# Kernel optimization log

Measured on AMD Instinct MI355X. Metric: run time of the kernel, lower is better.

The kernel has to match this reference:

```python
import jax, jax.numpy as jnp
import numpy as np

B, L, H, Di, N, K, R = 2, 512, 2048, 4096, 16, 4, 128


def setup_inputs() -> dict:
    key = jax.random.key(0)
    ks = jax.random.split(key, 8)
    s = 0.02
    inp = {
        "x": jax.random.normal(ks[0], (B, L, H), jnp.float32),
        "in_w": jax.random.normal(ks[1], (2 * Di, H), jnp.float32) * s,
        "in_b": jnp.zeros((2 * Di,), jnp.float32),
        "conv_w": jax.random.normal(ks[2], (Di, 1, K), jnp.float32) * s,  # depthwise conv weight
        "conv_b": jnp.zeros((Di,), jnp.float32),
        "xproj_w": jax.random.normal(ks[3], (R + 2 * N, Di), jnp.float32) * s,
        "dt_w": jax.random.normal(ks[4], (Di, R), jnp.float32) * s,
        "dt_b": jax.random.normal(ks[5], (Di,), jnp.float32) * 0.1,
        "A_log": jnp.log(jnp.broadcast_to(jnp.arange(1, N + 1, dtype=jnp.float32)[None, :], (Di, N))) + jnp.zeros((Di, N), jnp.float32),
        "D": jnp.ones((Di,), jnp.float32),
        "out_w": jax.random.normal(ks[6], (H, Di), jnp.float32) * s,
        "out_b": jnp.zeros((H,), jnp.float32),
    }
    return inp


def reference(x, in_w, in_b, conv_w, conv_b, xproj_w, dt_w, dt_b, A_log, D, out_w, out_b):
    silu = jax.nn.silu
    # in_proj -> split into hidden path and gate
    proj = x @ in_w.T + in_b                       # [B, L, 2*Di]
    h, gate = jnp.split(proj, 2, axis=-1)          # each [B, L, Di]
    # causal depthwise conv1d over time
    hc = jnp.transpose(h, (0, 2, 1))               # [B, Di, L]
    hc = jax.lax.conv_general_dilated(
        hc, conv_w, window_strides=(1,), padding=[(K - 1, 0)],
        dimension_numbers=("NCH", "OIH", "NCH"), feature_group_count=Di)
    hc = silu(hc + conv_b[None, :, None])          # [B, Di, L]
    hs = jnp.transpose(hc, (0, 2, 1))              # [B, L, Di]
    # input-dependent SSM parameters
    sp = hs @ xproj_w.T                            # [B, L, R + 2N]
    ts, Bm, Cm = sp[..., :R], sp[..., R:R + N], sp[..., R + N:]
    dt = jax.nn.softplus(ts @ dt_w.T + dt_b)       # [B, L, Di]
    A = -jnp.exp(A_log)                            # [Di, N]
    dA = jnp.exp(dt[..., None] * A[None, None])    # [B, L, Di, N]
    dBu = dt[..., None] * Bm[:, :, None, :] * hs[..., None]  # [B, L, Di, N]

    # selective scan: s_t = dA_t * s_{t-1} + dBu_t ; y_t = s_t . C_t
    def step(s, inputs):
        dA_t, dBu_t, C_t = inputs                  # [B,Di,N], [B,Di,N], [B,N]
        s = dA_t * s + dBu_t
        y = jnp.einsum("bdn,bn->bd", s, C_t)
        return s, y

    s0 = jnp.zeros((x.shape[0], Di, N), x.dtype)
    _, ys = jax.lax.scan(step, s0, (jnp.swapaxes(dA, 0, 1), jnp.swapaxes(dBu, 0, 1), jnp.swapaxes(Cm, 0, 1)))
    y = jnp.transpose(ys, (1, 0, 2))               # [B, L, Di]
    y = (y + hs * D) * silu(gate)
    return y @ out_w.T + out_b                     # [B, L, H]
```

## Files before the change

### kernel.cpp

```cpp
#include <hip/hip_runtime.h>
#include <hip/hip_bf16.h>

typedef __hip_bfloat16 bf16;
typedef _Float16 fp16;
typedef short bf16x8 __attribute__((ext_vector_type(8)));
typedef float f32x4 __attribute__((ext_vector_type(4)));
typedef _Float16 half8 __attribute__((ext_vector_type(8)));

#define BB 2
#define LL 512
#define HH 2048
#define DI 4096
#define NST 16
#define KK 4
#define RR 128
#define BLM (BB*LL)
#define CN 16
#define LC (LL/CN)
#define ZXP 16
#define ZOUT 4

enum { MODE_PROJ = 0, MODE_XPROJ = 1, MODE_DT = 2, MODE_OUT = 3 };

__device__ __forceinline__ float sigmoidf_(float x) { return 1.f / (1.f + __expf(-x)); }
__device__ __forceinline__ float softplusf_(float x) {
    return fmaxf(x, 0.f) + log1pf(__expf(-fabsf(x)));
}
__device__ __forceinline__ unsigned int bfpack(float a, float b) {
    __hip_bfloat162 h = __float22bfloat162_rn(make_float2(a, b));
    union { __hip_bfloat162 h; unsigned int u; } cv; cv.h = h;
    return cv.u;
}

typedef const __attribute__((address_space(1))) unsigned int* gas_t;
typedef __attribute__((address_space(3))) unsigned int* las_t;
__device__ __forceinline__ void gld16(const void* g, void* l) {
    __builtin_amdgcn_global_load_lds((gas_t)g, (las_t)l, 16, 0, 0);
}

__device__ __forceinline__ void cvt_seg(const float* s, bf16* d, int i) {
    float4 v = ((const float4*)s)[i];
    uint2 o; o.x = bfpack(v.x, v.y); o.y = bfpack(v.z, v.w);
    ((uint2*)d)[i] = o;
}

__global__ __launch_bounds__(256) void cvt_all(
    const float* __restrict__ s0, bf16* __restrict__ d0, int n0,
    const float* __restrict__ s1, bf16* __restrict__ d1, int n1,
    const float* __restrict__ s2, bf16* __restrict__ d2, int n2,
    const float* __restrict__ s3, bf16* __restrict__ d3, int n3)
{
    int i = blockIdx.x * 256 + threadIdx.x;
    int stride = gridDim.x * 256;
    int t1 = n0 + n1, t2 = t1 + n2, t3 = t2 + n3;
    for (; i < t3; i += stride) {
        if      (i < n0) cvt_seg(s0, d0, i);
        else if (i < t1) cvt_seg(s1, d1, i - n0);
        else if (i < t2) cvt_seg(s2, d2, i - t1);
        else             cvt_seg(s3, d3, i - t2);
    }
}

__global__ __launch_bounds__(256) void cvt_f32_bf16(
    const float* __restrict__ src, bf16* __restrict__ dst, int n4)
{
    int i = blockIdx.x * 256 + threadIdx.x;
    int stride = gridDim.x * 256;
    for (; i < n4; i += stride) cvt_seg(src, dst, i);
}

template<int BM, int BN, int MODE>
__global__ __launch_bounds__(256) void gemm_bf16(
    const bf16* __restrict__ A, const bf16* __restrict__ Bw,
    int N, int K, int lda, int ldb,
    const float* __restrict__ bias,
    float* __restrict__ outf, bf16* __restrict__ outh, bf16* __restrict__ outh2,
    fp16* __restrict__ s0, fp16* __restrict__ s1,
    fp16* __restrict__ s2, fp16* __restrict__ s3)
{
    __shared__ short sA[BM * 32];
    __shared__ short sB[BN * 32];
    const int tid = threadIdx.x;
    const int col0 = blockIdx.x * BN;
    const int row0 = blockIdx.y * BM;
    const int wave = tid >> 6;
    const int lane = tid & 63;
    constexpr int NJ = (BM == 64 || BN == 64) ? 2 : 4;
    const int wr = (BM == 128) ? ((wave >> 1) * 64) : 0;
    const int wc = (BM == 64) ? (wave * 32) : ((wave & 1) * (BN / 2));
    const int lr = lane & 15;
    const int kq = (lane >> 4) << 3;

    const int kpb = K / gridDim.z;
    const int kbeg = blockIdx.z * kpb;
    const int kend = kbeg + kpb;

    const int r0 = tid >> 2;
    const int kc = (tid & 3) << 3;

    f32x4 acc[4][NJ] = {};

    for (int k0 = kbeg; k0 < kend; k0 += 32) {
        #pragma unroll
        for (int p = 0; p < BM / 64; p++) {
            int r = r0 + p * 64;
            gld16(A + (size_t)(row0 + r) * lda + k0 + kc, &sA[r * 32 + kc]);
        }
        #pragma unroll
        for (int p = 0; p < BN / 64; p++) {
            int rr = r0 + p * 64;
            int nb = col0 + rr; if (nb > N - 1) nb = N - 1;
            gld16(Bw + (size_t)nb * ldb + k0 + kc, &sB[rr * 32 + kc]);
        }
        __syncthreads();
        bf16x8 af[4], bfr[NJ];
        #pragma unroll
        for (int i = 0; i < 4; i++)
            af[i] = *(const bf16x8*)(&sA[(wr + i * 16 + lr) * 32 + kq]);
        #pragma unroll
        for (int j = 0; j < NJ; j++)
            bfr[j] = *(const bf16x8*)(&sB[(wc + j * 16 + lr) * 32 + kq]);
        #pragma unroll
        for (int i = 0; i < 4; i++)
            #pragma unroll
            for (int j = 0; j < NJ; j++)
                acc[i][j] = __builtin_amdgcn_mfma_f32_16x16x32_bf16(af[i], bfr[j], acc[i][j], 0, 0, 0);
        __syncthreads();
    }

    fp16* oslice = nullptr;
    if (MODE == MODE_OUT) {
        int z = blockIdx.z;
        oslice = (z == 0) ? s0 : (z == 1) ? s1 : (z == 2) ? s2 : s3;
    }
    const int drow = (lane >> 4) << 2;
    const int dcol = lane & 15;
    #pragma unroll
    for (int i = 0; i < 4; i++) {
        #pragma unroll
        for (int j = 0; j < NJ; j++) {
            int n = col0 + wc + j * 16 + dcol;
            if (n >= N) continue;
            float bv = bias ? bias[n] : 0.f;
            #pragma unroll
            for (int r = 0; r < 4; r++) {
                int m = row0 + wr + i * 16 + drow + r;
                float v = acc[i][j][r];
                if (MODE == MODE_PROJ) {
                    v += bv;
                    if (n < DI) outh2[(size_t)m * DI + n] = (bf16)v;
                    else        outh[(size_t)m * DI + (n - DI)] = (bf16)v;
                } else if (MODE == MODE_XPROJ) {
                    outf[(size_t)blockIdx.z * (BLM * 160) + (size_t)m * 160 + n] = v;
                } else if (MODE == MODE_DT) {
                    outf[(size_t)m * DI + n] = softplusf_(v + bv);
                } else {
                    oslice[(size_t)m * HH + n] = (fp16)v;
                }
            }
        }
    }
}

__global__ __launch_bounds__(256) void reduce_sp(
    const float* __restrict__ spS, float* __restrict__ sp_f, bf16* __restrict__ ts_b)
{
    int i = blockIdx.x * 256 + threadIdx.x;
    int row = i / 40, c4 = (i % 40) * 4;
    float4 s = make_float4(0.f, 0.f, 0.f, 0.f);
    #pragma unroll
    for (int z = 0; z < ZXP; z++) {
        float4 v = *(const float4*)&spS[(size_t)z * (BLM * 160) + (size_t)row * 160 + c4];
        s.x += v.x; s.y += v.y; s.z += v.z; s.w += v.w;
    }
    *(float4*)&sp_f[(size_t)row * 160 + c4] = s;
    if (c4 < RR) {
        uint2 o; o.x = bfpack(s.x, s.y); o.y = bfpack(s.z, s.w);
        *(uint2*)&ts_b[(size_t)row * RR + c4] = o;
    }
}

__global__ __launch_bounds__(256) void reduce_out(
    const fp16* __restrict__ s0, const fp16* __restrict__ s1,
    const fp16* __restrict__ s2, const fp16* __restrict__ s3,
    const float* __restrict__ bias, float* __restrict__ out)
{
    int i = blockIdx.x * 256 + threadIdx.x;
    int c8 = (i & 255) << 3;
    half8 a = ((const half8*)s0)[i];
    half8 b = ((const half8*)s1)[i];
    half8 c = ((const half8*)s2)[i];
    half8 d = ((const half8*)s3)[i];
    float r[8];
    #pragma unroll
    for (int e = 0; e < 8; e++)
        r[e] = (float)a[e] + (float)b[e] + (float)c[e] + (float)d[e] + bias[c8 + e];
    ((float4*)out)[2 * i]     = make_float4(r[0], r[1], r[2], r[3]);
    ((float4*)out)[2 * i + 1] = make_float4(r[4], r[5], r[6], r[7]);
}

__global__ __launch_bounds__(256) void conv_silu(
    const bf16* __restrict__ h, const float* __restrict__ conv_w,
    const float* __restrict__ conv_b, bf16* __restrict__ hs_b)
{
    int idx = blockIdx.x * 256 + threadIdx.x;
    int d = idx & (DI - 1);
    int l = (idx >> 12) & (LL - 1);
    float acc = conv_b[d];
    #pragma unroll
    for (int k = 0; k < KK; k++) {
        int ls = l - (KK - 1) + k;
        if (ls >= 0) acc += (float)h[(size_t)idx + (size_t)(ls - l) * DI] * conv_w[d * KK + k];
    }
    float s = acc * sigmoidf_(acc);
    hs_b[idx] = (bf16)s;
}

__global__ __launch_bounds__(256) void scan_part1(
    const float* __restrict__ dtr, const float* __restrict__ sp,
    const bf16* __restrict__ hs_b, const float* __restrict__ A_log,
    float* __restrict__ P_ws, float* __restrict__ S_ws)
{
    int bid = blockIdx.x;
    int c  = bid & (CN - 1);
    int db = (bid >> 4) & (DI / 256 - 1);
    int b  = bid >> 8;
    int d  = db * 256 + threadIdx.x;

    float A[NST], P[NST], S[NST];
    #pragma unroll
    for (int n = 0; n < NST; n++) {
        A[n] = -__expf(A_log[d * NST + n]);
        P[n] = 1.f; S[n] = 0.f;
    }
    const float* spb = sp + (size_t)b * LL * 160;
    size_t base = (size_t)b * LL * DI + d;
    for (int l = c * LC; l < (c + 1) * LC; l++) {
        size_t off = base + (size_t)l * DI;
        float dtv = dtr[off];
        float hsv = (float)hs_b[off];
        float dh = dtv * hsv;
        #pragma unroll
        for (int n = 0; n < NST; n++) {
            float a  = __expf(dtv * A[n]);
            float Bn = spb[l * 160 + RR + n];
            S[n] = a * S[n] + dh * Bn;
            P[n] *= a;
        }
    }
    size_t o = ((size_t)((b * CN + c) * DI) + d) * NST;
    #pragma unroll
    for (int q = 0; q < 4; q++) {
        *(float4*)&P_ws[o + q * 4] = make_float4(P[q*4], P[q*4+1], P[q*4+2], P[q*4+3]);
        *(float4*)&S_ws[o + q * 4] = make_float4(S[q*4], S[q*4+1], S[q*4+2], S[q*4+3]);
    }
}

__global__ __launch_bounds__(256) void scan_part2(
    const float* __restrict__ dtr, const float* __restrict__ sp,
    const bf16* __restrict__ hs_b, const bf16* __restrict__ g_b,
    const float* __restrict__ A_log, const float* __restrict__ Dv,
    const float* __restrict__ P_ws, const float* __restrict__ S_ws,
    bf16* __restrict__ y_b)
{
    int bid = blockIdx.x;
    int c  = bid & (CN - 1);
    int db = (bid >> 4) & (DI / 256 - 1);
    int b  = bid >> 8;
    int d  = db * 256 + threadIdx.x;

    float s[NST];
    #pragma unroll
    for (int n = 0; n < NST; n++) s[n] = 0.f;
    for (int j = 0; j < c; j++) {
        size_t o = ((size_t)((b * CN + j) * DI) + d) * NST;
        #pragma unroll
        for (int q = 0; q < 4; q++) {
            float4 Pq = *(const float4*)&P_ws[o + q * 4];
            float4 Sq = *(const float4*)&S_ws[o + q * 4];
            s[q*4+0] = Pq.x * s[q*4+0] + Sq.x;
            s[q*4+1] = Pq.y * s[q*4+1] + Sq.y;
            s[q*4+2] = Pq.z * s[q*4+2] + Sq.z;
            s[q*4+3] = Pq.w * s[q*4+3] + Sq.w;
        }
    }

    float A[NST];
    #pragma unroll
    for (int n = 0; n < NST; n++) A[n] = -__expf(A_log[d * NST + n]);
    float Dd = Dv[d];

    const float* spb = sp + (size_t)b * LL * 160;
    size_t base = (size_t)b * LL * DI + d;
    for (int l = c * LC; l < (c + 1) * LC; l++) {
        size_t off = base + (size_t)l * DI;
        float dtv = dtr[off];
        float hsv = (float)hs_b[off];
        float dh = dtv * hsv;
        float y = 0.f;
        #pragma unroll
        for (int n = 0; n < NST; n++) {
            float a  = __expf(dtv * A[n]);
            float Bn = spb[l * 160 + RR + n];
            float Cn = spb[l * 160 + RR + NST + n];
            s[n] = a * s[n] + dh * Bn;
            y += s[n] * Cn;
        }
        float gv = (float)g_b[off];
        y_b[off] = (bf16)((y + hsv * Dd) * (gv * sigmoidf_(gv)));
    }
}

extern "C" void kernel_launch(void* const* d_in, const int* in_sizes, int n_in,
                              void* d_out, int out_size, void* d_ws, size_t ws_size,
                              hipStream_t stream)
{
    const float* x       = (const float*)d_in[0];
    const float* in_w    = (const float*)d_in[1];
    const float* in_b    = (const float*)d_in[2];
    const float* conv_w  = (const float*)d_in[3];
    const float* conv_b  = (const float*)d_in[4];
    const float* xproj_w = (const float*)d_in[5];
    const float* dt_w    = (const float*)d_in[6];
    const float* dt_b    = (const float*)d_in[7];
    const float* A_log   = (const float*)d_in[8];
    const float* Dv      = (const float*)d_in[9];
    const float* out_w   = (const float*)d_in[10];
    const float* out_b   = (const float*)d_in[11];
    float* out = (float*)d_out;

    char* ws = (char*)d_ws;
    const size_t MB = 1u << 20;
    bf16*  x_b    = (bf16*)(ws);
    float* spS    = (float*)(ws);
    float* P_ws   = (float*)(ws);
    float* S_ws   = (float*)(ws + 8 * MB);
    fp16*  oS2    = (fp16*)(ws);
    fp16*  oS3    = (fp16*)(ws + 4 * MB);
    bf16*  in_w_b = (bf16*)(ws + 16 * MB);
    bf16*  y_b    = (bf16*)(ws + 16 * MB);
    bf16*  hs_b   = (bf16*)(ws + 24 * MB);
    fp16*  oS0    = (fp16*)(ws + 24 * MB);
    fp16*  oS1    = (fp16*)(ws + 28 * MB);
    float* dt_f   = (float*)(ws + 32 * MB);
    bf16*  ow_b   = (bf16*)(ws + 32 * MB);
    bf16*  h_b    = (bf16*)(ws + 48 * MB);
    bf16*  g_b    = (bf16*)(ws + 56 * MB);
    char* p = ws + 64 * MB;
    float* sp_f = (float*)p; p += (size_t)BLM * 160 * 4;
    bf16*  ts_b = (bf16*)p;  p += (size_t)BLM * RR * 2;
    bf16*  xw_b = (bf16*)p;  p += (size_t)(RR + 2 * NST) * DI * 2;
    bf16*  dtw_b= (bf16*)p;  p += (size_t)DI * RR * 2;

    cvt_all<<<2048, 256, 0, stream>>>(
        x, x_b, BLM * HH / 4,
        in_w, in_w_b, 2 * DI * HH / 4,
        xproj_w, xw_b, (RR + 2 * NST) * DI / 4,
        dt_w, dtw_b, DI * RR / 4);
    gemm_bf16<128, 64, MODE_PROJ><<<dim3((2 * DI) / 64, BLM / 128, 1), 256, 0, stream>>>(
        x_b, in_w_b, 2 * DI, HH, HH, HH, in_b, nullptr, g_b, h_b,
        nullptr, nullptr, nullptr, nullptr);
    conv_silu<<<(BLM * DI) / 256, 256, 0, stream>>>(h_b, conv_w, conv_b, hs_b);
    gemm_bf16<64, 128, MODE_XPROJ><<<dim3(2, BLM / 64, ZXP), 256, 0, stream>>>(
        hs_b, xw_b, RR + 2 * NST, DI, DI, DI, nullptr, spS, nullptr, nullptr,
        nullptr, nullptr, nullptr, nullptr);
    reduce_sp<<<160, 256, 0, stream>>>(spS, sp_f, ts_b);
    gemm_bf16<64, 128, MODE_DT><<<dim3(DI / 128, BLM / 64, 1), 256, 0, stream>>>(
        ts_b, dtw_b, DI, RR, RR, RR, dt_b, dt_f, nullptr, nullptr,
        nullptr, nullptr, nullptr, nullptr);
    scan_part1<<<BB * (DI / 256) * CN, 256, 0, stream>>>(
        dt_f, sp_f, hs_b, A_log, P_ws, S_ws);
    scan_part2<<<BB * (DI / 256) * CN, 256, 0, stream>>>(
        dt_f, sp_f, hs_b, g_b, A_log, Dv, P_ws, S_ws, y_b);
    cvt_f32_bf16<<<512, 256, 0, stream>>>(out_w, ow_b, HH * DI / 4);
    gemm_bf16<128, 64, MODE_OUT><<<dim3(HH / 64, BLM / 128, ZOUT), 256, 0, stream>>>(
        y_b, ow_b, HH, DI, DI, DI, nullptr, nullptr, nullptr, nullptr,
        oS0, oS1, oS2, oS3);
    reduce_out<<<1024, 256, 0, stream>>>(oS0, oS1, oS2, oS3, out_b, out);
}
```

Measured before the change: 368.3 us.

## Store dt and x-proj partials in fp16, fuse out_w cast into conv

The dt projection output and the split-K x_proj partial sums are now stored as fp16 instead of fp32, which halves their global traffic; reduce_sp is widened to 8-element fp16 loads. The out_w fp32->bf16 conversion is merged into the conv+SiLU kernel as one grid-stride kernel, removing a launch. The scan chunk-state buffers are moved from a d-major to an n-major layout so that per-n writes and reads coalesce across threads. The workspace is reshuffled to fit the new buffers. Storing dt in fp16 lowers precision in the scan input, and the fused kernel's grid-stride loop may reduce the parallelism available to the conv.

```diff
diff --git a/kernel.cpp b/kernel.cpp
--- a/kernel.cpp
+++ b/kernel.cpp
@@ -19,6 +19,8 @@
 #define LC (LL/CN)
 #define ZXP 16
 #define ZOUT 4
+#define CONV_N (BLM*DI)
+#define CVT4_N (HH*DI/4)
 
 enum { MODE_PROJ = 0, MODE_XPROJ = 1, MODE_DT = 2, MODE_OUT = 3 };
 
@@ -61,20 +63,12 @@
     }
 }
 
-__global__ __launch_bounds__(256) void cvt_f32_bf16(
-    const float* __restrict__ src, bf16* __restrict__ dst, int n4)
-{
-    int i = blockIdx.x * 256 + threadIdx.x;
-    int stride = gridDim.x * 256;
-    for (; i < n4; i += stride) cvt_seg(src, dst, i);
-}
-
 template<int BM, int BN, int MODE>
 __global__ __launch_bounds__(256) void gemm_bf16(
     const bf16* __restrict__ A, const bf16* __restrict__ Bw,
     int N, int K, int lda, int ldb,
     const float* __restrict__ bias,
-    float* __restrict__ outf, bf16* __restrict__ outh, bf16* __restrict__ outh2,
+    bf16* __restrict__ outh, bf16* __restrict__ outh2,
     fp16* __restrict__ s0, fp16* __restrict__ s1,
     fp16* __restrict__ s2, fp16* __restrict__ s3)
 {
@@ -128,7 +122,7 @@
         __syncthreads();
     }
 
-    fp16* oslice = nullptr;
+    fp16* oslice = s0;
     if (MODE == MODE_OUT) {
         int z = blockIdx.z;
         oslice = (z == 0) ? s0 : (z == 1) ? s1 : (z == 2) ? s2 : s3;
@@ -151,9 +145,9 @@
                     if (n < DI) outh2[(size_t)m * DI + n] = (bf16)v;
                     else        outh[(size_t)m * DI + (n - DI)] = (bf16)v;
                 } else if (MODE == MODE_XPROJ) {
-                    outf[(size_t)blockIdx.z * (BLM * 160) + (size_t)m * 160 + n] = v;
+                    s0[(size_t)blockIdx.z * (BLM * 160) + (size_t)m * 160 + n] = (fp16)v;
                 } else if (MODE == MODE_DT) {
-                    outf[(size_t)m * DI + n] = softplusf_(v + bv);
+                    s0[(size_t)m * DI + n] = (fp16)softplusf_(v + bv);
                 } else {
                     oslice[(size_t)m * HH + n] = (fp16)v;
                 }
@@ -162,21 +156,50 @@
     }
 }
 
+__global__ __launch_bounds__(256) void conv_cvtow(
+    const bf16* __restrict__ h, const float* __restrict__ conv_w,
+    const float* __restrict__ conv_b, bf16* __restrict__ hs_b,
+    const float* __restrict__ ow, bf16* __restrict__ ow_b)
+{
+    int i = blockIdx.x * 256 + threadIdx.x;
+    int stride = gridDim.x * 256;
+    for (; i < CONV_N + CVT4_N; i += stride) {
+        if (i < CONV_N) {
+            int idx = i;
+            int d = idx & (DI - 1);
+            int l = (idx >> 12) & (LL - 1);
+            float acc = conv_b[d];
+            #pragma unroll
+            for (int k = 0; k < KK; k++) {
+                int ls = l - (KK - 1) + k;
+                if (ls >= 0) acc += (float)h[(size_t)idx + (size_t)(ls - l) * DI] * conv_w[d * KK + k];
+            }
+            float s = acc * sigmoidf_(acc);
+            hs_b[idx] = (bf16)s;
+        } else {
+            cvt_seg(ow, ow_b, i - CONV_N);
+        }
+    }
+}
+
 __global__ __launch_bounds__(256) void reduce_sp(
-    const float* __restrict__ spS, float* __restrict__ sp_f, bf16* __restrict__ ts_b)
+    const fp16* __restrict__ spS, float* __restrict__ sp_f, bf16* __restrict__ ts_b)
 {
     int i = blockIdx.x * 256 + threadIdx.x;
-    int row = i / 40, c4 = (i % 40) * 4;
-    float4 s = make_float4(0.f, 0.f, 0.f, 0.f);
+    int row = i / 20, c8 = (i % 20) * 8;
+    float r[8] = {};
     #pragma unroll
     for (int z = 0; z < ZXP; z++) {
-        float4 v = *(const float4*)&spS[(size_t)z * (BLM * 160) + (size_t)row * 160 + c4];
-        s.x += v.x; s.y += v.y; s.z += v.z; s.w += v.w;
-    }
-    *(float4*)&sp_f[(size_t)row * 160 + c4] = s;
-    if (c4 < RR) {
-        uint2 o; o.x = bfpack(s.x, s.y); o.y = bfpack(s.z, s.w);
-        *(uint2*)&ts_b[(size_t)row * RR + c4] = o;
+        half8 v = *(const half8*)&spS[(size_t)z * (BLM * 160) + (size_t)row * 160 + c8];
+        #pragma unroll
+        for (int e = 0; e < 8; e++) r[e] += (float)v[e];
+    }
+    *(float4*)&sp_f[(size_t)row * 160 + c8]     = make_float4(r[0], r[1], r[2], r[3]);
+    *(float4*)&sp_f[(size_t)row * 160 + c8 + 4] = make_float4(r[4], r[5], r[6], r[7]);
+    if (c8 < RR) {
+        uint4 o = make_uint4(bfpack(r[0], r[1]), bfpack(r[2], r[3]),
+                             bfpack(r[4], r[5]), bfpack(r[6], r[7]));
+        *(uint4*)&ts_b[(size_t)row * RR + c8] = o;
     }
 }
 
@@ -199,25 +222,8 @@
     ((float4*)out)[2 * i + 1] = make_float4(r[4], r[5], r[6], r[7]);
 }
 
-__global__ __launch_bounds__(256) void conv_silu(
-    const bf16* __restrict__ h, const float* __restrict__ conv_w,
-    const float* __restrict__ conv_b, bf16* __restrict__ hs_b)
-{
-    int idx = blockIdx.x * 256 + threadIdx.x;
-    int d = idx & (DI - 1);
-    int l = (idx >> 12) & (LL - 1);
-    float acc = conv_b[d];
-    #pragma unroll
-    for (int k = 0; k < KK; k++) {
-        int ls = l - (KK - 1) + k;
-        if (ls >= 0) acc += (float)h[(size_t)idx + (size_t)(ls - l) * DI] * conv_w[d * KK + k];
-    }
-    float s = acc * sigmoidf_(acc);
-    hs_b[idx] = (bf16)s;
-}
-
 __global__ __launch_bounds__(256) void scan_part1(
-    const float* __restrict__ dtr, const float* __restrict__ sp,
+    const fp16* __restrict__ dtr, const float* __restrict__ sp,
     const bf16* __restrict__ hs_b, const float* __restrict__ A_log,
     float* __restrict__ P_ws, float* __restrict__ S_ws)
 {
@@ -237,7 +243,7 @@
     size_t base = (size_t)b * LL * DI + d;
     for (int l = c * LC; l < (c + 1) * LC; l++) {
         size_t off = base + (size_t)l * DI;
-        float dtv = dtr[off];
+        float dtv = (float)dtr[off];
         float hsv = (float)hs_b[off];
         float dh = dtv * hsv;
         #pragma unroll
@@ -248,16 +254,16 @@
             P[n] *= a;
         }
     }
-    size_t o = ((size_t)((b * CN + c) * DI) + d) * NST;
-    #pragma unroll
-    for (int q = 0; q < 4; q++) {
-        *(float4*)&P_ws[o + q * 4] = make_float4(P[q*4], P[q*4+1], P[q*4+2], P[q*4+3]);
-        *(float4*)&S_ws[o + q * 4] = make_float4(S[q*4], S[q*4+1], S[q*4+2], S[q*4+3]);
+    size_t ob = (size_t)(b * CN + c) * NST * DI + d;
+    #pragma unroll
+    for (int n = 0; n < NST; n++) {
+        P_ws[ob + (size_t)n * DI] = P[n];
+        S_ws[ob + (size_t)n * DI] = S[n];
     }
 }
 
 __global__ __launch_bounds__(256) void scan_part2(
-    const float* __restrict__ dtr, const float* __restrict__ sp,
+    const fp16* __restrict__ dtr, const float* __restrict__ sp,
     const bf16* __restrict__ hs_b, const bf16* __restrict__ g_b,
     const float* __restrict__ A_log, const float* __restrict__ Dv,
     const float* __restrict__ P_ws, const float* __restrict__ S_ws,
@@ -273,16 +279,10 @@
     #pragma unroll
     for (int n = 0; n < NST; n++) s[n] = 0.f;
     for (int j = 0; j < c; j++) {
-        size_t o = ((size_t)((b * CN + j) * DI) + d) * NST;
-        #pragma unroll
-        for (int q = 0; q < 4; q++) {
-            float4 Pq = *(const float4*)&P_ws[o + q * 4];
-            float4 Sq = *(const float4*)&S_ws[o + q * 4];
-            s[q*4+0] = Pq.x * s[q*4+0] + Sq.x;
-            s[q*4+1] = Pq.y * s[q*4+1] + Sq.y;
-            s[q*4+2] = Pq.z * s[q*4+2] + Sq.z;
-            s[q*4+3] = Pq.w * s[q*4+3] + Sq.w;
-        }
+        size_t ojb = (size_t)(b * CN + j) * NST * DI + d;
+        #pragma unroll
+        for (int n = 0; n < NST; n++)
+            s[n] = P_ws[ojb + (size_t)n * DI] * s[n] + S_ws[ojb + (size_t)n * DI];
     }
 
     float A[NST];
@@ -294,7 +294,7 @@
     size_t base = (size_t)b * LL * DI + d;
     for (int l = c * LC; l < (c + 1) * LC; l++) {
         size_t off = base + (size_t)l * DI;
-        float dtv = dtr[off];
+        float dtv = (float)dtr[off];
         float hsv = (float)hs_b[off];
         float dh = dtv * hsv;
         float y = 0.f;
@@ -331,20 +331,20 @@
 
     char* ws = (char*)d_ws;
     const size_t MB = 1u << 20;
-    bf16*  x_b    = (bf16*)(ws);
-    float* spS    = (float*)(ws);
+    bf16*  h_b    = (bf16*)(ws);
+    fp16*  spS    = (fp16*)(ws);
     float* P_ws   = (float*)(ws);
+    fp16*  oS0    = (fp16*)(ws);
+    fp16*  oS1    = (fp16*)(ws + 4 * MB);
+    bf16*  x_b    = (bf16*)(ws + 8 * MB);
     float* S_ws   = (float*)(ws + 8 * MB);
-    fp16*  oS2    = (fp16*)(ws);
-    fp16*  oS3    = (fp16*)(ws + 4 * MB);
+    fp16*  oS2    = (fp16*)(ws + 8 * MB);
+    fp16*  oS3    = (fp16*)(ws + 12 * MB);
     bf16*  in_w_b = (bf16*)(ws + 16 * MB);
-    bf16*  y_b    = (bf16*)(ws + 16 * MB);
-    bf16*  hs_b   = (bf16*)(ws + 24 * MB);
-    fp16*  oS0    = (fp16*)(ws + 24 * MB);
-    fp16*  oS1    = (fp16*)(ws + 28 * MB);
-    float* dt_f   = (float*)(ws + 32 * MB);
-    bf16*  ow_b   = (bf16*)(ws + 32 * MB);
-    bf16*  h_b    = (bf16*)(ws + 48 * MB);
+    bf16*  ow_b   = (bf16*)(ws + 16 * MB);
+    bf16*  y_b    = (bf16*)(ws + 32 * MB);
+    fp16*  dt_h   = (fp16*)(ws + 40 * MB);
+    bf16*  hs_b   = (bf16*)(ws + 48 * MB);
     bf16*  g_b    = (bf16*)(ws + 56 * MB);
     char* p = ws + 64 * MB;
     float* sp_f = (float*)p; p += (size_t)BLM * 160 * 4;
@@ -358,23 +358,22 @@
         xproj_w, xw_b, (RR + 2 * NST) * DI / 4,
         dt_w, dtw_b, DI * RR / 4);
     gemm_bf16<128, 64, MODE_PROJ><<<dim3((2 * DI) / 64, BLM / 128, 1), 256, 0, stream>>>(
-        x_b, in_w_b, 2 * DI, HH, HH, HH, in_b, nullptr, g_b, h_b,
+        x_b, in_w_b, 2 * DI, HH, HH, HH, in_b, g_b, h_b,
         nullptr, nullptr, nullptr, nullptr);
-    conv_silu<<<(BLM * DI) / 256, 256, 0, stream>>>(h_b, conv_w, conv_b, hs_b);
+    conv_cvtow<<<2048, 256, 0, stream>>>(h_b, conv_w, conv_b, hs_b, out_w, ow_b);
     gemm_bf16<64, 128, MODE_XPROJ><<<dim3(2, BLM / 64, ZXP), 256, 0, stream>>>(
-        hs_b, xw_b, RR + 2 * NST, DI, DI, DI, nullptr, spS, nullptr, nullptr,
-        nullptr, nullptr, nullptr, nullptr);
-    reduce_sp<<<160, 256, 0, stream>>>(spS, sp_f, ts_b);
+        hs_b, xw_b, RR + 2 * NST, DI, DI, DI, nullptr, nullptr, nullptr,
+        spS, nullptr, nullptr, nullptr);
+    reduce_sp<<<80, 256, 0, stream>>>(spS, sp_f, ts_b);
     gemm_bf16<64, 128, MODE_DT><<<dim3(DI / 128, BLM / 64, 1), 256, 0, stream>>>(
-        ts_b, dtw_b, DI, RR, RR, RR, dt_b, dt_f, nullptr, nullptr,
-        nullptr, nullptr, nullptr, nullptr);
+        ts_b, dtw_b, DI, RR, RR, RR, dt_b, nullptr, nullptr,
+        dt_h, nullptr, nullptr, nullptr);
     scan_part1<<<BB * (DI / 256) * CN, 256, 0, stream>>>(
-        dt_f, sp_f, hs_b, A_log, P_ws, S_ws);
+        dt_h, sp_f, hs_b, A_log, P_ws, S_ws);
     scan_part2<<<BB * (DI / 256) * CN, 256, 0, stream>>>(
-        dt_f, sp_f, hs_b, g_b, A_log, Dv, P_ws, S_ws, y_b);
-    cvt_f32_bf16<<<512, 256, 0, stream>>>(out_w, ow_b, HH * DI / 4);
+        dt_h, sp_f, hs_b, g_b, A_log, Dv, P_ws, S_ws, y_b);
     gemm_bf16<128, 64, MODE_OUT><<<dim3(HH / 64, BLM / 128, ZOUT), 256, 0, stream>>>(
-        y_b, ow_b, HH, DI, DI, DI, nullptr, nullptr, nullptr, nullptr,
+        y_b, ow_b, HH, DI, DI, DI, nullptr, nullptr, nullptr,
         oS0, oS1, oS2, oS3);
     reduce_out<<<1024, 256, 0, stream>>>(oS0, oS1, oS2, oS3, out_b, out);
 }
```

New measurement: 364.4 us. About the same (-1.1%).
